# Optimization experiments

Measured on AMD Instinct MI355X. Metric: run time of the kernel, lower is better.

The kernel has to match this reference:

```python
import jax, jax.numpy as jnp
import numpy as np

S = 32            # state: nodes per graph, conv output channels
B = 4096          # number of graphs
N = B * S         # total nodes
E = 2 * 1024 * 1024  # total edges (avg degree 16)
A = 2             # action_space_dimension
NACT = 32         # number_of_actions (adv heads)
EPS = 1e-5


def setup_inputs() -> dict:
    key = jax.random.key(0)
    ks = jax.random.split(key, 24)
    f = lambda k, sh, s: (jax.random.normal(k, sh, jnp.float32) * s)
    return {
        'x': f(ks[0], (N, 2), 1.0),
        'edge_index': jax.random.randint(ks[1], (2, E), 0, N),
        # conv1 MLP: Linear(4,16) -> ReLU -> Linear(16,S)
        'c1W1': f(ks[2], (4, 16), 0.5), 'c1b1': jnp.zeros((16,), jnp.float32),
        'c1W2': f(ks[3], (16, S), 0.25), 'c1b2': jnp.zeros((S,), jnp.float32),
        # conv2/conv3 MLPs: Linear(2*S,16) -> ReLU -> Linear(16,S)
        'c2W1': f(ks[4], (2 * S, 16), 0.12), 'c2b1': jnp.zeros((16,), jnp.float32),
        'c2W2': f(ks[5], (16, S), 0.25), 'c2b2': jnp.zeros((S,), jnp.float32),
        'c3W1': f(ks[6], (2 * S, 16), 0.12), 'c3b1': jnp.zeros((16,), jnp.float32),
        'c3W2': f(ks[7], (16, S), 0.25), 'c3b2': jnp.zeros((S,), jnp.float32),
        # 3 BatchNorm1d(S) layers (stacked)
        'bn_g': jnp.ones((3, S), jnp.float32), 'bn_b': jnp.zeros((3, S), jnp.float32),
        # dense head MLP 1024->256->256->256
        'mW1': f(ks[8], (S * S, 256), 0.03), 'mb1': jnp.zeros((256,), jnp.float32),
        'mW2': f(ks[9], (256, 256), 0.06), 'mb2': jnp.zeros((256,), jnp.float32),
        'mW3': f(ks[10], (256, 256), 0.06), 'mb3': jnp.zeros((256,), jnp.float32),
        # dueling heads
        'vW': f(ks[11], (256, 1), 0.06), 'vb': jnp.zeros((1,), jnp.float32),
        'aW': f(ks[12], (NACT, 256, A), 0.06), 'ab': jnp.zeros((NACT, A), jnp.float32),
    }


def _edgeconv(x, src, dst, W1, b1, W2, b2):
    # PyG EdgeConv with aggr='add': msg = MLP(cat[x_i, x_j - x_i]), summed at target i
    xi = x[dst]                       # [E, F]
    xj = x[src]                       # [E, F]
    m = jnp.concatenate([xi, xj - xi], axis=-1)        # [E, 2F]
    h = jnp.maximum(m @ W1 + b1, 0.0) @ W2 + b2        # [E, S]
    return jax.ops.segment_sum(h, dst, num_segments=x.shape[0])  # [N, S]


def _bn(h, g, b):
    # BatchNorm1d in training mode: batch stats over node dim, biased variance
    mu = h.mean(axis=0)
    var = jnp.mean((h - mu) ** 2, axis=0)
    return (h - mu) * jax.lax.rsqrt(var + EPS) * g + b


def reference(x, edge_index, c1W1, c1b1, c1W2, c1b2, c2W1, c2b1, c2W2, c2b2,
              c3W1, c3b1, c3W2, c3b2, bn_g, bn_b, mW1, mb1, mW2, mb2,
              mW3, mb3, vW, vb, aW, ab):
    src, dst = edge_index[0], edge_index[1]
    h = _edgeconv(x, src, dst, c1W1, c1b1, c1W2, c1b2)
    h = jax.nn.relu(_bn(h, bn_g[0], bn_b[0]))
    h = _edgeconv(h, src, dst, c2W1, c2b1, c2W2, c2b2)
    h = jax.nn.relu(_bn(h, bn_g[1], bn_b[1]))
    h = _edgeconv(h, src, dst, c3W1, c3b1, c3W2, c3b2)
    h = jax.nn.relu(_bn(h, bn_g[2], bn_b[2]))
    nb = x.shape[0] // S                                 # graphs in batch
    out = h.reshape(nb, S * S)                           # [B, in_size]
    out = jax.nn.relu(out @ mW1 + mb1)
    out = jax.nn.relu(out @ mW2 + mb2)
    out = jax.nn.relu(out @ mW3 + mb3)                   # [B, 256]
    value = out @ vW + vb                                # [B, 1]
    adv = jnp.einsum('bf,nfa->bna', out, aW) + ab        # [B, NACT, A]
    q = value[:, :, None] + adv - adv.mean(axis=2, keepdims=True)
    return q
```

## Files before the change

### kernel.cpp

```cpp
#include <hip/hip_runtime.h>
#include <hip/hip_fp16.h>

#define NN 131072
#define EE 2097152
#define SS 32
#define HH 16
#define BB 4096
#define EPS 1e-5f

#define BKT 512
#define BNODES 256
#define CAP 4864
#define SCAP 8192
#define TILE 8192

typedef _Float16 f16x8 __attribute__((ext_vector_type(8)));
typedef float f32x4 __attribute__((ext_vector_type(4)));

__global__ __launch_bounds__(1024) void k_bsort(const int* __restrict__ ei, int* __restrict__ gcount,
                                                int* __restrict__ words) {
    __shared__ int cnt[BKT];
    __shared__ int tstart[BKT];
    __shared__ int gshift[BKT];
    __shared__ int sc[BKT];
    __shared__ int sword[TILE];
    __shared__ int sdst[TILE];
    int t = threadIdx.x;
    if (t < BKT) cnt[t] = 0;
    __syncthreads();
    int e0 = blockIdx.x * TILE;
#pragma unroll
    for (int it = 0; it < TILE / 1024; ++it) {
        int dst = ei[EE + e0 + it * 1024 + t];
        atomicAdd(&cnt[dst >> 8], 1);
    }
    __syncthreads();
    int val = (t < BKT) ? cnt[t] : 0;
    if (t < BKT) sc[t] = val;
    __syncthreads();
    for (int d = 1; d < BKT; d <<= 1) {
        int v2 = (t >= d && t < BKT) ? sc[t - d] : 0;
        __syncthreads();
        if (t < BKT) sc[t] += v2;
        __syncthreads();
    }
    if (t < BKT) {
        int excl = sc[t] - val;
        tstart[t] = excl;
        gshift[t] = t * CAP + atomicAdd(&gcount[t], val) - excl;
        cnt[t] = 0;
    }
    __syncthreads();
#pragma unroll
    for (int it = 0; it < TILE / 1024; ++it) {
        int e = e0 + it * 1024 + t;
        int src = ei[e];
        int dst = ei[EE + e];
        int b = dst >> 8;
        int r = atomicAdd(&cnt[b], 1);
        int p = tstart[b] + r;
        sword[p] = src | ((dst & 255) << 17);
        sdst[p] = gshift[b] + p;
    }
    __syncthreads();
#pragma unroll
    for (int it = 0; it < TILE / 1024; ++it) {
        int i = it * 1024 + t;
        words[sdst[i]] = sword[i];
    }
}

__global__ __launch_bounds__(512) void k_csr(const int* __restrict__ words, const int* __restrict__ gcount,
                                             int* __restrict__ ssrc, int* __restrict__ offs,
                                             int* __restrict__ offe) {
    __shared__ int hist[BNODES];
    __shared__ int sc[BNODES];
    __shared__ int base[BNODES];
    int t = threadIdx.x;
    int b = blockIdx.x;
    if (t < BNODES) hist[t] = 0;
    __syncthreads();
    int cnt = gcount[b];
    const int* wp = words + (size_t)b * CAP;
    for (int p = t; p < cnt; p += 512) atomicAdd(&hist[wp[p] >> 17], 1);
    __syncthreads();
    int val = 0, pval = 0;
    if (t < BNODES) {
        val = hist[t];
        pval = (val + 15) & ~15;
        sc[t] = pval;
    }
    __syncthreads();
    for (int d = 1; d < BNODES; d <<= 1) {
        int v2 = (t >= d && t < BNODES) ? sc[t - d] : 0;
        __syncthreads();
        if (t < BNODES) sc[t] += v2;
        __syncthreads();
    }
    int gbase = b * SCAP;
    if (t < BNODES) {
        base[t] = sc[t] - pval;
        offs[b * BNODES + t] = gbase + base[t];
        offe[b * BNODES + t] = gbase + base[t] + val;
        hist[t] = 0;
    }
    __syncthreads();
    for (int p = t; p < cnt; p += 512) {
        int w = wp[p];
        int dl = w >> 17;
        int r = atomicAdd(&hist[dl], 1);
        ssrc[gbase + base[dl] + r] = w & 0x1FFFF;
    }
    if (t < BNODES) {
        int s = gbase + base[t];
        for (int i = val; i < pval; ++i) ssrc[s + i] = NN;
    }
}

__global__ __launch_bounds__(256) void k_prep(const float* __restrict__ mW1, const float* __restrict__ mW2,
                                              const float* __restrict__ mW3, const float* __restrict__ vW,
                                              const float* __restrict__ vb, const float* __restrict__ aW,
                                              const float* __restrict__ ab,
                                              _Float16* __restrict__ W1T, _Float16* __restrict__ W2T,
                                              _Float16* __restrict__ W3T, _Float16* __restrict__ BqT,
                                              float* __restrict__ biasq, int* __restrict__ gcount,
                                              float* __restrict__ bns) {
    int i = blockIdx.x * 256 + threadIdx.x;
    {
        int k = i >> 8, n = i & 255;
        W1T[(size_t)n * 1024 + k] = (_Float16)mW1[i];
    }
    if (i < 65536) {
        int k = i >> 8, n = i & 255;
        W2T[n * 256 + k] = (_Float16)mW2[i];
        W3T[n * 256 + k] = (_Float16)mW3[i];
    }
    if (i < 16384) {
        int f = i >> 6, j = i & 63;
        int n = j >> 1, a = j & 1;
        float wa = aW[n * 512 + f * 2 + a];
        float wo = aW[n * 512 + f * 2 + (1 - a)];
        BqT[j * 256 + f] = (_Float16)(vW[f] + 0.5f * (wa - wo));
    }
    if (i < 64) biasq[i] = vb[0] + 0.5f * (ab[i] - ab[i ^ 1]);
    if (i < 512) gcount[i] = 0;
    if (i < 192) bns[i] = 0.f;
}

__global__ __launch_bounds__(256) void k_pre1(const float* __restrict__ x, const float* __restrict__ W1,
                                              const float* __restrict__ b1, float* __restrict__ u,
                                              __half* __restrict__ v) {
    int t = blockIdx.x * 256 + threadIdx.x;
    int n = t >> 4, c = t & 15;
    float x0 = x[n * 2], x1 = x[n * 2 + 1];
    float w0 = W1[c], w1 = W1[16 + c], w2 = W1[32 + c], w3 = W1[48 + c];
    u[t] = b1[c] + x0 * (w0 - w2) + x1 * (w1 - w3);
    v[t] = __float2half(x0 * w2 + x1 * w3);
    if (blockIdx.x == 0 && t < 16) v[NN * 16 + t] = __float2half(-60000.0f);
}

__global__ __launch_bounds__(256) void k_bnpre(const float* __restrict__ y, const float* __restrict__ bns,
                                               const float* __restrict__ g, const float* __restrict__ bb,
                                               const float* __restrict__ W1, const float* __restrict__ b1,
                                               float* __restrict__ u, __half* __restrict__ v) {
    __shared__ float sh[16][33];
    __shared__ float wd[32][16];
    __shared__ float wv[32][16];
    __shared__ float scL[32], soL[32];
    int t = threadIdx.x;
    if (t < 32) {
        const float inv_n = 1.0f / (float)NN;
        float mean = bns[t] * inv_n;
        float var = bns[32 + t] * inv_n - mean * mean;
        float s = g[t] * rsqrtf(var + EPS);
        scL[t] = s;
        soL[t] = bb[t] - mean * s;
    }
    for (int i = t; i < 512; i += 256) {
        int f = i >> 4, c = i & 15;
        float wt = W1[i];
        float wb = W1[512 + i];
        wd[f][c] = wt - wb;
        wv[f][c] = wb;
    }
    __syncthreads();
    int nb = blockIdx.x * 16;
    for (int i = t; i < 512; i += 256) {
        int col = i & 31;
        sh[i >> 5][col] = fmaxf(y[nb * 32 + i] * scL[col] + soL[col], 0.f);
    }
    __syncthreads();
    int c = t & 15, nl = t >> 4;
    float uu = b1[c], vv = 0.f;
#pragma unroll
    for (int f = 0; f < 32; ++f) {
        float hv = sh[nl][f];
        uu += hv * wd[f][c];
        vv += hv * wv[f][c];
    }
    int n = nb + nl;
    u[n * 16 + c] = uu;
    v[n * 16 + c] = __float2half(vv);
    if (blockIdx.x == 0 && t < 16) v[NN * 16 + t] = __float2half(-60000.0f);
}

__global__ __launch_bounds__(256) void k_gather(const float* __restrict__ u, const __half* __restrict__ v,
                                                const int* __restrict__ ssrc, const int* __restrict__ offs,
                                                const int* __restrict__ offe,
                                                const float* __restrict__ W2, const float* __restrict__ b2,
                                                float* __restrict__ y) {
    __shared__ float sw2[512];
    __shared__ float sagg[32 * 18];
    __shared__ float cntL[32];
    int t = threadIdx.x;
    float w2a = W2[t], w2b = W2[t + 256];
    float b2r0 = b2[(t & 7) * 4], b2r1 = b2[(t & 7) * 4 + 1];
    float b2r2 = b2[(t & 7) * 4 + 2], b2r3 = b2[(t & 7) * 4 + 3];
    int nl = t >> 3, c2 = t & 7;
    int n = blockIdx.x * 32 + nl;
    int s0 = offs[n], e0 = offe[n];
    int pe = s0 + ((e0 - s0 + 15) & ~15);
    float2 uc = *(const float2*)(u + (size_t)n * 16 + 2 * c2);
    float a0 = 0.f, a1 = 0.f;
    for (int p = s0; p < pe; p += 16) {
        int idx[16];
#pragma unroll
        for (int i = 0; i < 16; ++i) idx[i] = ssrc[p + i];
        float2 vv[16];
#pragma unroll
        for (int i = 0; i < 16; ++i)
            vv[i] = __half22float2(*(const __half2*)(v + (size_t)idx[i] * 16 + 2 * c2));
#pragma unroll
        for (int i = 0; i < 16; ++i) {
            a0 += fmaxf(uc.x + vv[i].x, 0.f);
            a1 += fmaxf(uc.y + vv[i].y, 0.f);
        }
    }
    sagg[nl * 18 + 2 * c2] = a0;
    sagg[nl * 18 + 2 * c2 + 1] = a1;
    if (c2 == 0) cntL[nl] = (float)(e0 - s0);
    sw2[t] = w2a;
    sw2[t + 256] = w2b;
    __syncthreads();
    int node = t >> 3, oc = (t & 7) * 4;
    float cw = cntL[node];
    float o0 = b2r0 * cw, o1 = b2r1 * cw, o2 = b2r2 * cw, o3 = b2r3 * cw;
#pragma unroll
    for (int k = 0; k < 16; ++k) {
        float a = sagg[node * 18 + k];
        o0 += a * sw2[k * 32 + oc];
        o1 += a * sw2[k * 32 + oc + 1];
        o2 += a * sw2[k * 32 + oc + 2];
        o3 += a * sw2[k * 32 + oc + 3];
    }
    *(float4*)(y + (size_t)(blockIdx.x * 32 + node) * 32 + oc) = make_float4(o0, o1, o2, o3);
}

__global__ __launch_bounds__(256) void k_bnstat2(const float* __restrict__ y, float* __restrict__ bns) {
    __shared__ float ssm[8][33];
    __shared__ float ssq[8][33];
    int t = threadIdx.x;
    int c = t & 31, g = t >> 5;
    size_t r0 = (size_t)blockIdx.x * 512;
    float sm = 0.f, sq = 0.f;
    for (int i = 0; i < 64; ++i) {
        float val = y[(r0 + g + (size_t)i * 8) * 32 + c];
        sm += val;
        sq += val * val;
    }
    ssm[g][c] = sm;
    ssq[g][c] = sq;
    __syncthreads();
    if (t < 32) {
        float a = 0.f, bq = 0.f;
#pragma unroll
        for (int gg = 0; gg < 8; ++gg) { a += ssm[gg][t]; bq += ssq[gg][t]; }
        atomicAdd(&bns[t], a);
        atomicAdd(&bns[32 + t], bq);
    }
}

__global__ __launch_bounds__(256) void k_bnrelu16(const float* __restrict__ y, const float* __restrict__ bns,
                                                  const float* __restrict__ g, const float* __restrict__ bb,
                                                  _Float16* __restrict__ h16) {
    int t = blockIdx.x * 256 + threadIdx.x;
    int j = t & 31;
    const float inv_n = 1.0f / (float)NN;
    float mean = bns[j] * inv_n;
    float var = bns[32 + j] * inv_n - mean * mean;
    float sc = g[j] * rsqrtf(var + EPS);
    float sh = bb[j] - mean * sc;
    h16[t] = (_Float16)fmaxf(y[t] * sc + sh, 0.f);
}

__global__ __launch_bounds__(256) void k_mgemm(const _Float16* __restrict__ A, const _Float16* __restrict__ BT,
                                               const float* __restrict__ bias, float* __restrict__ Cf,
                                               _Float16* __restrict__ Ch, int M, int N, int K,
                                               int relu, int out16) {
    int tid = threadIdx.x;
    int w = tid >> 6, l = tid & 63, q = l >> 4, r = l & 15;
    int rowBase = blockIdx.x * 64;
    int col = blockIdx.y * 64 + w * 16 + r;
    const _Float16* ap = A + (size_t)(rowBase + r) * K + q * 8;
    const _Float16* bp = BT + (size_t)col * K + q * 8;
    f32x4 z = {0.f, 0.f, 0.f, 0.f};
    f32x4 acc[4] = {z, z, z, z};
    for (int k0 = 0; k0 < K; k0 += 32) {
        f16x8 bf = *(const f16x8*)(bp + k0);
        f16x8 a0 = *(const f16x8*)(ap + k0);
        f16x8 a1 = *(const f16x8*)(ap + k0 + (size_t)16 * K);
        f16x8 a2 = *(const f16x8*)(ap + k0 + (size_t)32 * K);
        f16x8 a3 = *(const f16x8*)(ap + k0 + (size_t)48 * K);
        acc[0] = __builtin_amdgcn_mfma_f32_16x16x32_f16(a0, bf, acc[0], 0, 0, 0);
        acc[1] = __builtin_amdgcn_mfma_f32_16x16x32_f16(a1, bf, acc[1], 0, 0, 0);
        acc[2] = __builtin_amdgcn_mfma_f32_16x16x32_f16(a2, bf, acc[2], 0, 0, 0);
        acc[3] = __builtin_amdgcn_mfma_f32_16x16x32_f16(a3, bf, acc[3], 0, 0, 0);
    }
    float bv = bias[col];
#pragma unroll
    for (int rt = 0; rt < 4; ++rt) {
#pragma unroll
        for (int i = 0; i < 4; ++i) {
            int row = rowBase + rt * 16 + q * 4 + i;
            float val = acc[rt][i] + bv;
            if (relu) val = fmaxf(val, 0.f);
            if (out16) Ch[(size_t)row * N + col] = (_Float16)val;
            else       Cf[(size_t)row * N + col] = val;
        }
    }
}

extern "C" void kernel_launch(void* const* d_in, const int* in_sizes, int n_in,
                              void* d_out, int out_size, void* d_ws, size_t ws_size,
                              hipStream_t stream) {
    const float* x    = (const float*)d_in[0];
    const int*   ei   = (const int*)d_in[1];
    const float* c1W1 = (const float*)d_in[2];
    const float* c1b1 = (const float*)d_in[3];
    const float* c1W2 = (const float*)d_in[4];
    const float* c1b2 = (const float*)d_in[5];
    const float* c2W1 = (const float*)d_in[6];
    const float* c2b1 = (const float*)d_in[7];
    const float* c2W2 = (const float*)d_in[8];
    const float* c2b2 = (const float*)d_in[9];
    const float* c3W1 = (const float*)d_in[10];
    const float* c3b1 = (const float*)d_in[11];
    const float* c3W2 = (const float*)d_in[12];
    const float* c3b2 = (const float*)d_in[13];
    const float* bn_g = (const float*)d_in[14];
    const float* bn_b = (const float*)d_in[15];
    const float* mW1  = (const float*)d_in[16];
    const float* mb1  = (const float*)d_in[17];
    const float* mW2  = (const float*)d_in[18];
    const float* mb2  = (const float*)d_in[19];
    const float* mW3  = (const float*)d_in[20];
    const float* mb3  = (const float*)d_in[21];
    const float* vW   = (const float*)d_in[22];
    const float* vb   = (const float*)d_in[23];
    const float* aW   = (const float*)d_in[24];
    const float* ab   = (const float*)d_in[25];
    float* out = (float*)d_out;

    char* p = (char*)d_ws;
    auto take = [&](size_t bytes) {
        char* r = p;
        p += (bytes + 255) & ~(size_t)255;
        return r;
    };
    int*       gcount = (int*)take((size_t)BKT * 4);
    int*       words  = (int*)take((size_t)BKT * CAP * 4);
    int*       ssrc   = (int*)take((size_t)BKT * SCAP * 4);
    int*       offs   = (int*)take((size_t)NN * 4);
    int*       offe   = (int*)take((size_t)NN * 4);
    float*     u      = (float*)take((size_t)NN * HH * 4);
    __half*    v      = (__half*)take((size_t)(NN + 1) * HH * 2);
    float*     y      = (float*)take((size_t)NN * SS * 4);
    _Float16*  h16    = (_Float16*)take((size_t)NN * SS * 2);
    float*     bns    = (float*)take(3 * 64 * 4);
    _Float16*  W1T    = (_Float16*)take((size_t)256 * 1024 * 2);
    _Float16*  W2T    = (_Float16*)take((size_t)256 * 256 * 2);
    _Float16*  W3T    = (_Float16*)take((size_t)256 * 256 * 2);
    _Float16*  BqT    = (_Float16*)take((size_t)64 * 256 * 2);
    float*     biasq  = (float*)take(64 * 4);
    _Float16*  Xa     = (_Float16*)take((size_t)BB * 256 * 2);
    _Float16*  Xb     = (_Float16*)take((size_t)BB * 256 * 2);

    k_prep<<<1024, 256, 0, stream>>>(mW1, mW2, mW3, vW, vb, aW, ab,
                                     W1T, W2T, W3T, BqT, biasq, gcount, bns);

    k_bsort<<<EE / TILE, 1024, 0, stream>>>(ei, gcount, words);
    k_csr<<<BKT, 512, 0, stream>>>(words, gcount, ssrc, offs, offe);

    k_pre1<<<NN * 16 / 256, 256, 0, stream>>>(x, c1W1, c1b1, u, v);
    k_gather<<<NN / 32, 256, 0, stream>>>(u, v, ssrc, offs, offe, c1W2, c1b2, y);
    k_bnstat2<<<256, 256, 0, stream>>>(y, bns);
    k_bnpre<<<NN / 16, 256, 0, stream>>>(y, bns, bn_g, bn_b, c2W1, c2b1, u, v);
    k_gather<<<NN / 32, 256, 0, stream>>>(u, v, ssrc, offs, offe, c2W2, c2b2, y);
    k_bnstat2<<<256, 256, 0, stream>>>(y, bns + 64);
    k_bnpre<<<NN / 16, 256, 0, stream>>>(y, bns + 64, bn_g + 32, bn_b + 32, c3W1, c3b1, u, v);
    k_gather<<<NN / 32, 256, 0, stream>>>(u, v, ssrc, offs, offe, c3W2, c3b2, y);
    k_bnstat2<<<256, 256, 0, stream>>>(y, bns + 128);
    k_bnrelu16<<<NN * 32 / 256, 256, 0, stream>>>(y, bns + 128, bn_g + 64, bn_b + 64, h16);

    k_mgemm<<<dim3(BB / 64, 4), 256, 0, stream>>>(h16, W1T, mb1, nullptr, Xa, BB, 256, 1024, 1, 1);
    k_mgemm<<<dim3(BB / 64, 4), 256, 0, stream>>>(Xa, W2T, mb2, nullptr, Xb, BB, 256, 256, 1, 1);
    k_mgemm<<<dim3(BB / 64, 4), 256, 0, stream>>>(Xb, W3T, mb3, nullptr, Xa, BB, 256, 256, 1, 1);
    k_mgemm<<<dim3(BB / 64, 1), 256, 0, stream>>>(Xa, BqT, biasq, out, nullptr, BB, 64, 256, 0, 0);
}
```

Measured before the change: 332.5 us.

## Fuse BN statistics into gather, merge pre1 into prep, cache edge words in registers

Batch-norm sum and sum-of-squares are now accumulated inside the gather kernel using wave shuffles, shared atomics and 8-way striped global atomics, which removes three separate statistics passes over y. The first-layer u/v precompute is merged into the weight-prep kernel. The sort and CSR kernels keep loaded edge words in registers instead of re-reading them from global memory, and the final BN+ReLU kernel is vectorised to four elements per thread with shared scale/shift. In exchange there is more atomic contention in gather and higher register pressure in the CSR kernel, whose fixed 10-iteration loop assumes bucket counts at most 5120.

```diff
diff --git a/kernel.cpp b/kernel.cpp
--- a/kernel.cpp
+++ b/kernel.cpp
@@ -15,6 +15,7 @@
 #define TILE 8192
 
 typedef _Float16 f16x8 __attribute__((ext_vector_type(8)));
+typedef _Float16 f16x4 __attribute__((ext_vector_type(4)));
 typedef float f32x4 __attribute__((ext_vector_type(4)));
 
 __global__ __launch_bounds__(1024) void k_bsort(const int* __restrict__ ei, int* __restrict__ gcount,
@@ -29,10 +30,11 @@
     if (t < BKT) cnt[t] = 0;
     __syncthreads();
     int e0 = blockIdx.x * TILE;
+    int dreg[TILE / 1024];
 #pragma unroll
     for (int it = 0; it < TILE / 1024; ++it) {
-        int dst = ei[EE + e0 + it * 1024 + t];
-        atomicAdd(&cnt[dst >> 8], 1);
+        dreg[it] = ei[EE + e0 + it * 1024 + t];
+        atomicAdd(&cnt[dreg[it] >> 8], 1);
     }
     __syncthreads();
     int val = (t < BKT) ? cnt[t] : 0;
@@ -55,7 +57,7 @@
     for (int it = 0; it < TILE / 1024; ++it) {
         int e = e0 + it * 1024 + t;
         int src = ei[e];
-        int dst = ei[EE + e];
+        int dst = dreg[it];
         int b = dst >> 8;
         int r = atomicAdd(&cnt[b], 1);
         int p = tstart[b] + r;
@@ -82,7 +84,14 @@
     __syncthreads();
     int cnt = gcount[b];
     const int* wp = words + (size_t)b * CAP;
-    for (int p = t; p < cnt; p += 512) atomicAdd(&hist[wp[p] >> 17], 1);
+    int wreg[10];
+#pragma unroll
+    for (int it = 0; it < 10; ++it) {
+        int p = t + it * 512;
+        int w = (p < cnt) ? wp[p] : -1;
+        wreg[it] = w;
+        if (w >= 0) atomicAdd(&hist[w >> 17], 1);
+    }
     __syncthreads();
     int val = 0, pval = 0;
     if (t < BNODES) {
@@ -105,11 +114,14 @@
         hist[t] = 0;
     }
     __syncthreads();
-    for (int p = t; p < cnt; p += 512) {
-        int w = wp[p];
-        int dl = w >> 17;
-        int r = atomicAdd(&hist[dl], 1);
-        ssrc[gbase + base[dl] + r] = w & 0x1FFFF;
+#pragma unroll
+    for (int it = 0; it < 10; ++it) {
+        int w = wreg[it];
+        if (w >= 0) {
+            int dl = w >> 17;
+            int r = atomicAdd(&hist[dl], 1);
+            ssrc[gbase + base[dl] + r] = w & 0x1FFFF;
+        }
     }
     if (t < BNODES) {
         int s = gbase + base[t];
@@ -124,9 +136,19 @@
                                               _Float16* __restrict__ W1T, _Float16* __restrict__ W2T,
                                               _Float16* __restrict__ W3T, _Float16* __restrict__ BqT,
                                               float* __restrict__ biasq, int* __restrict__ gcount,
-                                              float* __restrict__ bns) {
+                                              float* __restrict__ bns,
+                                              const float* __restrict__ x, const float* __restrict__ c1W1,
+                                              const float* __restrict__ c1b1,
+                                              float* __restrict__ u, __half* __restrict__ v) {
     int i = blockIdx.x * 256 + threadIdx.x;
     {
+        int n = i >> 4, c = i & 15;
+        float x0 = x[n * 2], x1 = x[n * 2 + 1];
+        float w0 = c1W1[c], w1 = c1W1[16 + c], w2 = c1W1[32 + c], w3 = c1W1[48 + c];
+        u[i] = c1b1[c] + x0 * (w0 - w2) + x1 * (w1 - w3);
+        v[i] = __float2half(x0 * w2 + x1 * w3);
+    }
+    if (i < 262144) {
         int k = i >> 8, n = i & 255;
         W1T[(size_t)n * 1024 + k] = (_Float16)mW1[i];
     }
@@ -144,19 +166,8 @@
     }
     if (i < 64) biasq[i] = vb[0] + 0.5f * (ab[i] - ab[i ^ 1]);
     if (i < 512) gcount[i] = 0;
-    if (i < 192) bns[i] = 0.f;
-}
-
-__global__ __launch_bounds__(256) void k_pre1(const float* __restrict__ x, const float* __restrict__ W1,
-                                              const float* __restrict__ b1, float* __restrict__ u,
-                                              __half* __restrict__ v) {
-    int t = blockIdx.x * 256 + threadIdx.x;
-    int n = t >> 4, c = t & 15;
-    float x0 = x[n * 2], x1 = x[n * 2 + 1];
-    float w0 = W1[c], w1 = W1[16 + c], w2 = W1[32 + c], w3 = W1[48 + c];
-    u[t] = b1[c] + x0 * (w0 - w2) + x1 * (w1 - w3);
-    v[t] = __float2half(x0 * w2 + x1 * w3);
-    if (blockIdx.x == 0 && t < 16) v[NN * 16 + t] = __float2half(-60000.0f);
+    if (i < 1536) bns[i] = 0.f;
+    if (i < 16) v[NN * 16 + i] = __float2half(-60000.0f);
 }
 
 __global__ __launch_bounds__(256) void k_bnpre(const float* __restrict__ y, const float* __restrict__ bns,
@@ -169,12 +180,15 @@
     __shared__ float scL[32], soL[32];
     int t = threadIdx.x;
     if (t < 32) {
+        float sm = 0.f, sq = 0.f;
+#pragma unroll
+        for (int s = 0; s < 8; ++s) { sm += bns[s * 64 + t]; sq += bns[s * 64 + 32 + t]; }
         const float inv_n = 1.0f / (float)NN;
-        float mean = bns[t] * inv_n;
-        float var = bns[32 + t] * inv_n - mean * mean;
-        float s = g[t] * rsqrtf(var + EPS);
-        scL[t] = s;
-        soL[t] = bb[t] - mean * s;
+        float mean = sm * inv_n;
+        float var = sq * inv_n - mean * mean;
+        float s2 = g[t] * rsqrtf(var + EPS);
+        scL[t] = s2;
+        soL[t] = bb[t] - mean * s2;
     }
     for (int i = t; i < 512; i += 256) {
         int f = i >> 4, c = i & 15;
@@ -208,11 +222,14 @@
                                                 const int* __restrict__ ssrc, const int* __restrict__ offs,
                                                 const int* __restrict__ offe,
                                                 const float* __restrict__ W2, const float* __restrict__ b2,
-                                                float* __restrict__ y) {
+                                                float* __restrict__ y, float* __restrict__ bns) {
     __shared__ float sw2[512];
     __shared__ float sagg[32 * 18];
     __shared__ float cntL[32];
+    __shared__ float ssum[32];
+    __shared__ float ssq[32];
     int t = threadIdx.x;
+    if (t < 32) { ssum[t] = 0.f; ssq[t] = 0.f; }
     float w2a = W2[t], w2b = W2[t + 256];
     float b2r0 = b2[(t & 7) * 4], b2r1 = b2[(t & 7) * 4 + 1];
     float b2r2 = b2[(t & 7) * 4 + 2], b2r3 = b2[(t & 7) * 4 + 3];
@@ -254,43 +271,53 @@
         o3 += a * sw2[k * 32 + oc + 3];
     }
     *(float4*)(y + (size_t)(blockIdx.x * 32 + node) * 32 + oc) = make_float4(o0, o1, o2, o3);
-}
-
-__global__ __launch_bounds__(256) void k_bnstat2(const float* __restrict__ y, float* __restrict__ bns) {
-    __shared__ float ssm[8][33];
-    __shared__ float ssq[8][33];
-    int t = threadIdx.x;
-    int c = t & 31, g = t >> 5;
-    size_t r0 = (size_t)blockIdx.x * 512;
-    float sm = 0.f, sq = 0.f;
-    for (int i = 0; i < 64; ++i) {
-        float val = y[(r0 + g + (size_t)i * 8) * 32 + c];
-        sm += val;
-        sq += val * val;
-    }
-    ssm[g][c] = sm;
-    ssq[g][c] = sq;
-    __syncthreads();
-    if (t < 32) {
-        float a = 0.f, bq = 0.f;
-#pragma unroll
-        for (int gg = 0; gg < 8; ++gg) { a += ssm[gg][t]; bq += ssq[gg][t]; }
-        atomicAdd(&bns[t], a);
-        atomicAdd(&bns[32 + t], bq);
+    float q0 = o0 * o0, q1 = o1 * o1, q2 = o2 * o2, q3 = o3 * o3;
+#pragma unroll
+    for (int m = 8; m < 64; m <<= 1) {
+        o0 += __shfl_xor(o0, m); o1 += __shfl_xor(o1, m);
+        o2 += __shfl_xor(o2, m); o3 += __shfl_xor(o3, m);
+        q0 += __shfl_xor(q0, m); q1 += __shfl_xor(q1, m);
+        q2 += __shfl_xor(q2, m); q3 += __shfl_xor(q3, m);
+    }
+    if ((t & 63) < 8) {
+        atomicAdd(&ssum[oc], o0);     atomicAdd(&ssum[oc + 1], o1);
+        atomicAdd(&ssum[oc + 2], o2); atomicAdd(&ssum[oc + 3], o3);
+        atomicAdd(&ssq[oc], q0);      atomicAdd(&ssq[oc + 1], q1);
+        atomicAdd(&ssq[oc + 2], q2);  atomicAdd(&ssq[oc + 3], q3);
+    }
+    __syncthreads();
+    if (t < 64) {
+        float val = (t < 32) ? ssum[t] : ssq[t - 32];
+        atomicAdd(&bns[(blockIdx.x & 7) * 64 + t], val);
     }
 }
 
 __global__ __launch_bounds__(256) void k_bnrelu16(const float* __restrict__ y, const float* __restrict__ bns,
                                                   const float* __restrict__ g, const float* __restrict__ bb,
                                                   _Float16* __restrict__ h16) {
-    int t = blockIdx.x * 256 + threadIdx.x;
-    int j = t & 31;
-    const float inv_n = 1.0f / (float)NN;
-    float mean = bns[j] * inv_n;
-    float var = bns[32 + j] * inv_n - mean * mean;
-    float sc = g[j] * rsqrtf(var + EPS);
-    float sh = bb[j] - mean * sc;
-    h16[t] = (_Float16)fmaxf(y[t] * sc + sh, 0.f);
+    __shared__ float sc_[32], sh_[32];
+    int t = threadIdx.x;
+    if (t < 32) {
+        float sm = 0.f, sq = 0.f;
+#pragma unroll
+        for (int s = 0; s < 8; ++s) { sm += bns[s * 64 + t]; sq += bns[s * 64 + 32 + t]; }
+        const float inv_n = 1.0f / (float)NN;
+        float mean = sm * inv_n;
+        float var = sq * inv_n - mean * mean;
+        float sc = g[t] * rsqrtf(var + EPS);
+        sc_[t] = sc;
+        sh_[t] = bb[t] - mean * sc;
+    }
+    __syncthreads();
+    int i = (blockIdx.x * 256 + t) * 4;
+    float4 v4 = *(const float4*)(y + i);
+    int j = i & 31;
+    f16x4 o;
+    o[0] = (_Float16)fmaxf(v4.x * sc_[j] + sh_[j], 0.f);
+    o[1] = (_Float16)fmaxf(v4.y * sc_[j + 1] + sh_[j + 1], 0.f);
+    o[2] = (_Float16)fmaxf(v4.z * sc_[j + 2] + sh_[j + 2], 0.f);
+    o[3] = (_Float16)fmaxf(v4.w * sc_[j + 3] + sh_[j + 3], 0.f);
+    *(f16x4*)(h16 + i) = o;
 }
 
 __global__ __launch_bounds__(256) void k_mgemm(const _Float16* __restrict__ A, const _Float16* __restrict__ BT,
@@ -376,7 +403,7 @@
     __half*    v      = (__half*)take((size_t)(NN + 1) * HH * 2);
     float*     y      = (float*)take((size_t)NN * SS * 4);
     _Float16*  h16    = (_Float16*)take((size_t)NN * SS * 2);
-    float*     bns    = (float*)take(3 * 64 * 4);
+    float*     bns    = (float*)take(3 * 512 * 4);
     _Float16*  W1T    = (_Float16*)take((size_t)256 * 1024 * 2);
     _Float16*  W2T    = (_Float16*)take((size_t)256 * 256 * 2);
     _Float16*  W3T    = (_Float16*)take((size_t)256 * 256 * 2);
@@ -385,22 +412,19 @@
     _Float16*  Xa     = (_Float16*)take((size_t)BB * 256 * 2);
     _Float16*  Xb     = (_Float16*)take((size_t)BB * 256 * 2);
 
-    k_prep<<<1024, 256, 0, stream>>>(mW1, mW2, mW3, vW, vb, aW, ab,
-                                     W1T, W2T, W3T, BqT, biasq, gcount, bns);
+    k_prep<<<NN * 16 / 256, 256, 0, stream>>>(mW1, mW2, mW3, vW, vb, aW, ab,
+                                              W1T, W2T, W3T, BqT, biasq, gcount, bns,
+                                              x, c1W1, c1b1, u, v);
 
     k_bsort<<<EE / TILE, 1024, 0, stream>>>(ei, gcount, words);
     k_csr<<<BKT, 512, 0, stream>>>(words, gcount, ssrc, offs, offe);
 
-    k_pre1<<<NN * 16 / 256, 256, 0, stream>>>(x, c1W1, c1b1, u, v);
-    k_gather<<<NN / 32, 256, 0, stream>>>(u, v, ssrc, offs, offe, c1W2, c1b2, y);
-    k_bnstat2<<<256, 256, 0, stream>>>(y, bns);
+    k_gather<<<NN / 32, 256, 0, stream>>>(u, v, ssrc, offs, offe, c1W2, c1b2, y, bns);
     k_bnpre<<<NN / 16, 256, 0, stream>>>(y, bns, bn_g, bn_b, c2W1, c2b1, u, v);
-    k_gather<<<NN / 32, 256, 0, stream>>>(u, v, ssrc, offs, offe, c2W2, c2b2, y);
-    k_bnstat2<<<256, 256, 0, stream>>>(y, bns + 64);
-    k_bnpre<<<NN / 16, 256, 0, stream>>>(y, bns + 64, bn_g + 32, bn_b + 32, c3W1, c3b1, u, v);
-    k_gather<<<NN / 32, 256, 0, stream>>>(u, v, ssrc, offs, offe, c3W2, c3b2, y);
-    k_bnstat2<<<256, 256, 0, stream>>>(y, bns + 128);
-    k_bnrelu16<<<NN * 32 / 256, 256, 0, stream>>>(y, bns + 128, bn_g + 64, bn_b + 64, h16);
+    k_gather<<<NN / 32, 256, 0, stream>>>(u, v, ssrc, offs, offe, c2W2, c2b2, y, bns + 512);
+    k_bnpre<<<NN / 16, 256, 0, stream>>>(y, bns + 512, bn_g + 32, bn_b + 32, c3W1, c3b1, u, v);
+    k_gather<<<NN / 32, 256, 0, stream>>>(u, v, ssrc, offs, offe, c3W2, c3b2, y, bns + 1024);
+    k_bnrelu16<<<NN * 32 / 1024, 256, 0, stream>>>(y, bns + 1024, bn_g + 64, bn_b + 64, h16);
 
     k_mgemm<<<dim3(BB / 64, 4), 256, 0, stream>>>(h16, W1T, mb1, nullptr, Xa, BB, 256, 1024, 1, 1);
     k_mgemm<<<dim3(BB / 64, 4), 256, 0, stream>>>(Xa, W2T, mb2, nullptr, Xb, BB, 256, 256, 1, 1);
```

After: 307.0 us. -7.7%, faster.
